# Kernel optimization log

Measured on AMD Instinct MI355X. Metric: run time of the kernel, lower is better.

The kernel has to match this reference:

```python
import jax, jax.numpy as jnp
import numpy as np

N, E = 100000, 1600000
D_NODE, H, OUT = 64, 256, 256
NUM_LAYERS = 3


def setup_inputs() -> dict:
    key = jax.random.key(0)
    ks = jax.random.split(key, 12)
    s = lambda fan_in: 1.0 / np.sqrt(fan_in)
    return {
        "x": jax.random.normal(ks[0], (N, D_NODE), jnp.float32),
        "src": jax.random.randint(ks[1], (E,), 0, N, jnp.int32),
        "dst": jax.random.randint(ks[2], (E,), 0, N, jnp.int32),
        "w_node": jax.random.uniform(ks[3], (D_NODE, H), jnp.float32, -s(D_NODE), s(D_NODE)),
        "b_node": jnp.zeros((H,), jnp.float32),
        "w_gnn": jax.random.uniform(ks[4], (NUM_LAYERS, H, H), jnp.float32, -s(H), s(H)),
        "b_gnn": jnp.zeros((NUM_LAYERS, H), jnp.float32),
        "w_p1": jax.random.uniform(ks[5], (H, H), jnp.float32, -s(H), s(H)),
        "b_p1": jnp.zeros((H,), jnp.float32),
        "w_p2": jax.random.uniform(ks[6], (H, OUT), jnp.float32, -s(H), s(H)),
        "b_p2": jnp.zeros((OUT,), jnp.float32),
    }


def reference(x, src, dst, w_node, b_node, w_gnn, b_gnn, w_p1, b_p1, w_p2, b_p2):
    n = x.shape[0]
    # node projection
    h = x @ w_node + b_node  # [N, H]
    # per-dst neighbor counts (nodes with no neighbors keep zero message)
    deg = jax.ops.segment_sum(jnp.ones_like(dst, jnp.float32), dst, num_segments=n)
    denom = jnp.where(deg > 0, deg, 1.0)[:, None]  # [N, 1]
    for l in range(NUM_LAYERS):
        # scatter-mean aggregation of neighbor embeddings
        msg = jax.ops.segment_sum(h[src], dst, num_segments=n) / denom  # [N, H]
        h = jax.nn.relu(h + msg @ w_gnn[l] + b_gnn[l])
    g = h.mean(axis=0)  # [H]
    latent = jax.nn.relu(g @ w_p1 + b_p1) @ w_p2 + b_p2  # [OUT]
    return latent
```

## Files before the change

kernel.cpp:

```cpp
#include <hip/hip_runtime.h>
#include <hip/hip_bf16.h>
#include <cstdint>
#include <cstddef>

#define DNODE 64
#define HDIM 256
#define NLAYERS 3
#define NPART 8
#define CSH 13
#define HSLICES 128

typedef __attribute__((ext_vector_type(8))) short bf16x8;
typedef __attribute__((ext_vector_type(4))) float f32x4;

__device__ __forceinline__ ushort f2bf(float f) {
    __hip_bfloat16 b = __float2bfloat16(f);
    return *(ushort*)&b;
}
__device__ __forceinline__ float bf2f(ushort u) {
    return __uint_as_float((uint32_t)u << 16);
}
__device__ __forceinline__ unsigned char f2fp8(float f) {
    int p = __builtin_amdgcn_cvt_pk_fp8_f32(f, f, 0, false);
    return (unsigned char)(p & 0xFF);
}

__global__ __launch_bounds__(256) void k_pre(const int* __restrict__ esrc, const int* __restrict__ edst,
                                             int* __restrict__ deg2, int E, int histB, int npp, int nch,
                                             const float* __restrict__ x, ushort* __restrict__ xb, int n4, int xcB,
                                             const float* __restrict__ w_node, ushort* __restrict__ wnt,
                                             const float* __restrict__ w_gnn, ushort* __restrict__ wgt, int wcB,
                                             ushort* __restrict__ wct, float* __restrict__ bc,
                                             const float* __restrict__ b_node) {
    int b = blockIdx.x, tid = threadIdx.x;
    if (b < histB) {
        int part = b & (NPART - 1);
        int slice = b / NPART;
        int lo = part * npp, hi = lo + npp;
        int stride = HSLICES * 256;
        for (int e = slice * 256 + tid; e < E; e += stride) {
            int d = edst[e];
            int s = esrc[e];
            if (d >= lo && d < hi) atomicAdd(&deg2[(size_t)d * nch + (s >> CSH)], 1);
        }
    } else if (b < histB + xcB) {
        int i = (b - histB) * 256 + tid;
        if (i < n4) {
            float4 v = *(const float4*)&x[(size_t)i * 4];
            ushort4 o;
            o.x = f2bf(v.x); o.y = f2bf(v.y); o.z = f2bf(v.z); o.w = f2bf(v.w);
            *(ushort4*)&xb[(size_t)i * 4] = o;
        }
    } else if (b < histB + xcB + wcB) {
        int wb = b - histB - xcB;
        int n = tid;
        if (wb < DNODE / 16) {
            int k0 = wb * 16;
#pragma unroll
            for (int i = 0; i < 16; i++)
                wnt[(size_t)n * DNODE + k0 + i] = f2bf(w_node[(size_t)(k0 + i) * HDIM + n]);
        } else {
            wb -= DNODE / 16;
            int l = wb >> 4, k0 = (wb & 15) * 16;
            const float* s = w_gnn + (size_t)l * HDIM * HDIM;
            ushort* d = wgt + (size_t)l * HDIM * HDIM;
#pragma unroll
            for (int i = 0; i < 16; i++)
                d[(size_t)n * HDIM + k0 + i] = f2bf(s[(size_t)(k0 + i) * HDIM + n]);
        }
    } else {
        int k = b - histB - xcB - wcB;
        int n = tid;
        if (k < DNODE) {
            float s = 0.f;
            for (int j = 0; j < HDIM; j++) s = fmaf(w_node[(size_t)k * HDIM + j], w_gnn[(size_t)j * HDIM + n], s);
            wct[(size_t)n * DNODE + k] = f2bf(s);
        } else {
            float s = 0.f;
            for (int j = 0; j < HDIM; j++) s = fmaf(b_node[j], w_gnn[(size_t)j * HDIM + n], s);
            bc[n] = s;
        }
    }
}

__global__ __launch_bounds__(256) void k_scan_partial(const int* __restrict__ deg, int* __restrict__ bsum, int n) {
    __shared__ int sd[256];
    int tid = threadIdx.x;
    int base = blockIdx.x * 2048 + tid * 8;
    int s = 0;
#pragma unroll
    for (int j = 0; j < 8; j++) {
        int idx = base + j;
        if (idx < n) s += deg[idx];
    }
    sd[tid] = s;
    __syncthreads();
    for (int off = 128; off > 0; off >>= 1) {
        if (tid < off) sd[tid] += sd[tid + off];
        __syncthreads();
    }
    if (tid == 0) bsum[blockIdx.x] = sd[0];
}

__global__ __launch_bounds__(256) void k_scan_bsum(int* __restrict__ bsum, int nb) {
    __shared__ int ts[256];
    int tid = threadIdx.x;
    int v[4], loc[4];
    int s = 0;
#pragma unroll
    for (int j = 0; j < 4; j++) {
        int idx = tid * 4 + j;
        v[j] = (idx < nb) ? bsum[idx] : 0;
        loc[j] = s;
        s += v[j];
    }
    ts[tid] = s;
    __syncthreads();
    for (int off = 1; off < 256; off <<= 1) {
        int t = (tid >= off) ? ts[tid - off] : 0;
        __syncthreads();
        ts[tid] += t;
        __syncthreads();
    }
    int off0 = tid ? ts[tid - 1] : 0;
#pragma unroll
    for (int j = 0; j < 4; j++) {
        int idx = tid * 4 + j;
        if (idx < nb) bsum[idx] = off0 + loc[j];
    }
}

__global__ __launch_bounds__(256) void k_scan_final(const int* __restrict__ deg, const int* __restrict__ bsum,
                                                    int* __restrict__ rp2, int* __restrict__ cursor2,
                                                    int n, int Etot) {
    __shared__ int tsum[256];
    int tid = threadIdx.x;
    int base = blockIdx.x * 2048 + tid * 8;
    int loc[8];
    int s = 0;
#pragma unroll
    for (int j = 0; j < 8; j++) {
        int idx = base + j;
        int v = (idx < n) ? deg[idx] : 0;
        loc[j] = s;
        s += v;
    }
    tsum[tid] = s;
    __syncthreads();
    for (int off = 1; off < 256; off <<= 1) {
        int t = (tid >= off) ? tsum[tid - off] : 0;
        __syncthreads();
        tsum[tid] += t;
        __syncthreads();
    }
    int off0 = bsum[blockIdx.x] + (tid ? tsum[tid - 1] : 0);
#pragma unroll
    for (int j = 0; j < 8; j++) {
        int idx = base + j;
        if (idx < n) {
            int rp = off0 + loc[j];
            rp2[idx] = rp;
            cursor2[idx] = rp;
        }
    }
    if (blockIdx.x == 0 && tid == 0) rp2[n] = Etot;
}

__global__ __launch_bounds__(256) void k_fill_part(const int* __restrict__ esrc, const int* __restrict__ edst,
                                                   int* __restrict__ cursor2, int* __restrict__ colx,
                                                   int E, int npp, int nslices, int nch) {
    int part = blockIdx.x & (NPART - 1);
    int slice = blockIdx.x / NPART;
    int lo = part * npp;
    int hi = lo + npp;
    int stride = nslices * 256;
    for (int e = slice * 256 + (int)threadIdx.x; e < E; e += stride) {
        int d = edst[e];
        if (d >= lo && d < hi) {
            int s = esrc[e];
            int c = s >> CSH;
            int p = atomicAdd(&cursor2[(size_t)d * nch + c], 1);
            colx[p] = s;
        }
    }
}

__global__ __launch_bounds__(256) void k_proj(const ushort* __restrict__ xb,
                                              const ushort* __restrict__ wnt,
                                              const ushort* __restrict__ wct,
                                              const float* __restrict__ bn,
                                              const float* __restrict__ bc,
                                              ushort* __restrict__ hb,
                                              unsigned char* __restrict__ hw8,
                                              int M) {
    __shared__ ushort As[64][40];
    __shared__ ushort Bs[64][40];
    __shared__ ushort Cs[64][40];
    int tid = threadIdx.x;
    int w = tid >> 6, l = tid & 63;
    int row0 = blockIdx.y * 64, col0 = blockIdx.x * 64;
    int sr = tid >> 2, sc = (tid & 3) * 8;
    int wm = (w >> 1) * 32, wn_ = (w & 1) * 32;
    int fr = l & 15, fk = (l >> 4) * 8;
    f32x4 acch[2][2] = {};
    f32x4 accw[2][2] = {};

    for (int k0 = 0; k0 < DNODE; k0 += 32) {
        bf16x8 av = {0, 0, 0, 0, 0, 0, 0, 0};
        int gr = row0 + sr;
        if (gr < M) av = *(const bf16x8*)&xb[(size_t)gr * DNODE + k0 + sc];
        *(bf16x8*)&As[sr][sc] = av;
        *(bf16x8*)&Bs[sr][sc] = *(const bf16x8*)&wnt[(size_t)(col0 + sr) * DNODE + k0 + sc];
        *(bf16x8*)&Cs[sr][sc] = *(const bf16x8*)&wct[(size_t)(col0 + sr) * DNODE + k0 + sc];
        __syncthreads();
        bf16x8 af[2], bff[2], cf[2];
#pragma unroll
        for (int mi = 0; mi < 2; mi++) af[mi] = *(const bf16x8*)&As[wm + mi * 16 + fr][fk];
#pragma unroll
        for (int ni = 0; ni < 2; ni++) {
            bff[ni] = *(const bf16x8*)&Bs[wn_ + ni * 16 + fr][fk];
            cf[ni] = *(const bf16x8*)&Cs[wn_ + ni * 16 + fr][fk];
        }
#pragma unroll
        for (int mi = 0; mi < 2; mi++)
#pragma unroll
            for (int ni = 0; ni < 2; ni++) {
                acch[mi][ni] = __builtin_amdgcn_mfma_f32_16x16x32_bf16(af[mi], bff[ni], acch[mi][ni], 0, 0, 0);
                accw[mi][ni] = __builtin_amdgcn_mfma_f32_16x16x32_bf16(af[mi], cf[ni], accw[mi][ni], 0, 0, 0);
            }
        __syncthreads();
    }

#pragma unroll
    for (int ni = 0; ni < 2; ni++) {
        int gcol = col0 + wn_ + ni * 16 + fr;
        float bbh = bn[gcol];
        float bbw = bc[gcol];
#pragma unroll
        for (int mi = 0; mi < 2; mi++) {
#pragma unroll
            for (int j = 0; j < 4; j++) {
                int grow = row0 + wm + mi * 16 + (l >> 4) * 4 + j;
                if (grow >= M) continue;
                size_t idx = (size_t)grow * HDIM + gcol;
                hb[idx] = f2bf(acch[mi][ni][j] + bbh);
                hw8[idx] = f2fp8(accw[mi][ni][j] + bbw);
            }
        }
    }
}

__global__ __launch_bounds__(256) void k_gemm_hw(const ushort* __restrict__ A,
                                                 const ushort* __restrict__ Bt,
                                                 unsigned char* __restrict__ hw8,
                                                 int M) {
    __shared__ ushort As[64][40];
    __shared__ ushort Bs[64][40];
    int tid = threadIdx.x;
    int w = tid >> 6, l = tid & 63;
    int row0 = blockIdx.y * 64, col0 = blockIdx.x * 64;
    int sr = tid >> 2, sc = (tid & 3) * 8;
    int wm = (w >> 1) * 32, wn = (w & 1) * 32;
    int fr = l & 15, fk = (l >> 4) * 8;
    f32x4 acc[2][2] = {};

    for (int k0 = 0; k0 < HDIM; k0 += 32) {
        bf16x8 av = {0, 0, 0, 0, 0, 0, 0, 0};
        int gr = row0 + sr;
        if (gr < M) av = *(const bf16x8*)&A[(size_t)gr * HDIM + k0 + sc];
        *(bf16x8*)&As[sr][sc] = av;
        *(bf16x8*)&Bs[sr][sc] = *(const bf16x8*)&Bt[(size_t)(col0 + sr) * HDIM + k0 + sc];
        __syncthreads();
        bf16x8 af[2], bf[2];
#pragma unroll
        for (int mi = 0; mi < 2; mi++) af[mi] = *(const bf16x8*)&As[wm + mi * 16 + fr][fk];
#pragma unroll
        for (int ni = 0; ni < 2; ni++) bf[ni] = *(const bf16x8*)&Bs[wn + ni * 16 + fr][fk];
#pragma unroll
        for (int mi = 0; mi < 2; mi++)
#pragma unroll
            for (int ni = 0; ni < 2; ni++)
                acc[mi][ni] = __builtin_amdgcn_mfma_f32_16x16x32_bf16(af[mi], bf[ni], acc[mi][ni], 0, 0, 0);
        __syncthreads();
    }

#pragma unroll
    for (int ni = 0; ni < 2; ni++) {
        int gcol = col0 + wn + ni * 16 + fr;
#pragma unroll
        for (int mi = 0; mi < 2; mi++) {
#pragma unroll
            for (int j = 0; j < 4; j++) {
                int grow = row0 + wm + mi * 16 + (l >> 4) * 4 + j;
                if (grow >= M) continue;
                hw8[(size_t)grow * HDIM + gcol] = f2fp8(acc[mi][ni][j]);
            }
        }
    }
}

__device__ __forceinline__ void acc_fp8x16(uint4 v, float* acc) {
    uint32_t d[4] = {v.x, v.y, v.z, v.w};
#pragma unroll
    for (int i = 0; i < 4; i++) {
        auto lo = __builtin_amdgcn_cvt_pk_f32_fp8(d[i], false);
        auto hi = __builtin_amdgcn_cvt_pk_f32_fp8(d[i], true);
        acc[i * 4 + 0] += lo[0];
        acc[i * 4 + 1] += lo[1];
        acc[i * 4 + 2] += hi[0];
        acc[i * 4 + 3] += hi[1];
    }
}

__global__ __launch_bounds__(256) void k_agg(const unsigned char* __restrict__ hw8,
                                             const int* __restrict__ rp2,
                                             const int* __restrict__ colx,
                                             unsigned char* __restrict__ msg8, int N, int nch) {
    int tid = threadIdx.x;
    int node = blockIdx.x * 16 + (tid >> 4);
    if (node >= N) return;
    int f = tid & 15;
    int gbase = tid & 48;
    const unsigned char* hp = hw8 + (size_t)f * 16;

    int s = rp2[(size_t)node * nch];
    int e = rp2[(size_t)node * nch + nch];
    float acc[16] = {};

    for (int base = s; base < e; base += 16) {
        int rem = e - base;
        int cnt = rem > 16 ? 16 : rem;
        int cv = (f < cnt) ? colx[base + f] : 0;
        int t = 0;
        for (; t + 3 < cnt; t += 4) {
            int c0 = __shfl(cv, gbase + t);
            int c1 = __shfl(cv, gbase + t + 1);
            int c2 = __shfl(cv, gbase + t + 2);
            int c3 = __shfl(cv, gbase + t + 3);
            uint4 v0 = *(const uint4*)&hp[(size_t)c0 * HDIM];
            uint4 v1 = *(const uint4*)&hp[(size_t)c1 * HDIM];
            uint4 v2 = *(const uint4*)&hp[(size_t)c2 * HDIM];
            uint4 v3 = *(const uint4*)&hp[(size_t)c3 * HDIM];
            acc_fp8x16(v0, acc);
            acc_fp8x16(v1, acc);
            acc_fp8x16(v2, acc);
            acc_fp8x16(v3, acc);
        }
        for (; t < cnt; t++) {
            int c0 = __shfl(cv, gbase + t);
            uint4 v0 = *(const uint4*)&hp[(size_t)c0 * HDIM];
            acc_fp8x16(v0, acc);
        }
    }

    int d = e - s;
    float inv = 1.0f / (float)(d > 0 ? d : 1);
    uint32_t w0 = 0, w1 = 0, w2 = 0, w3 = 0;
    w0 = (uint32_t)__builtin_amdgcn_cvt_pk_fp8_f32(acc[0] * inv, acc[1] * inv, (int)w0, false);
    w0 = (uint32_t)__builtin_amdgcn_cvt_pk_fp8_f32(acc[2] * inv, acc[3] * inv, (int)w0, true);
    w1 = (uint32_t)__builtin_amdgcn_cvt_pk_fp8_f32(acc[4] * inv, acc[5] * inv, (int)w1, false);
    w1 = (uint32_t)__builtin_amdgcn_cvt_pk_fp8_f32(acc[6] * inv, acc[7] * inv, (int)w1, true);
    w2 = (uint32_t)__builtin_amdgcn_cvt_pk_fp8_f32(acc[8] * inv, acc[9] * inv, (int)w2, false);
    w2 = (uint32_t)__builtin_amdgcn_cvt_pk_fp8_f32(acc[10] * inv, acc[11] * inv, (int)w2, true);
    w3 = (uint32_t)__builtin_amdgcn_cvt_pk_fp8_f32(acc[12] * inv, acc[13] * inv, (int)w3, false);
    w3 = (uint32_t)__builtin_amdgcn_cvt_pk_fp8_f32(acc[14] * inv, acc[15] * inv, (int)w3, true);
    uint4 o = {w0, w1, w2, w3};
    *(uint4*)&msg8[(size_t)node * HDIM + f * 16] = o;
}

__global__ __launch_bounds__(256) void k_resid(ushort* __restrict__ hb, const unsigned char* __restrict__ msg8,
                                               const float* __restrict__ bias, int total8) {
    int stride = gridDim.x * 256;
    for (int i = blockIdx.x * 256 + (int)threadIdx.x; i < total8; i += stride) {
        int col0 = (i & 31) * 8;
        size_t off = (size_t)i * 8;
        bf16x8 h = *(const bf16x8*)&hb[off];
        uint2 m8 = *(const uint2*)&msg8[off];
        auto lo0 = __builtin_amdgcn_cvt_pk_f32_fp8(m8.x, false);
        auto hi0 = __builtin_amdgcn_cvt_pk_f32_fp8(m8.x, true);
        auto lo1 = __builtin_amdgcn_cvt_pk_f32_fp8(m8.y, false);
        auto hi1 = __builtin_amdgcn_cvt_pk_f32_fp8(m8.y, true);
        float mv[8] = {lo0[0], lo0[1], hi0[0], hi0[1], lo1[0], lo1[1], hi1[0], hi1[1]};
        float4 b0 = *(const float4*)&bias[col0];
        float4 b1 = *(const float4*)&bias[col0 + 4];
        float bl[8] = {b0.x, b0.y, b0.z, b0.w, b1.x, b1.y, b1.z, b1.w};
        ushort o[8];
#pragma unroll
        for (int k = 0; k < 8; k++)
            o[k] = f2bf(fmaxf(bf2f((ushort)h[k]) + mv[k] + bl[k], 0.f));
        *(uint4*)&hb[off] = *(uint4*)o;
    }
}

__global__ __launch_bounds__(256) void k_colsum_res(const ushort* __restrict__ hb,
                                                    const unsigned char* __restrict__ msg8,
                                                    const float* __restrict__ bias, float* __restrict__ g, int N) {
    __shared__ float cols[256];
    int tid = threadIdx.x;
    int f8 = tid & 31, r = tid >> 5;
    int col0 = f8 * 8;
    float4 b0 = *(const float4*)&bias[col0];
    float4 b1 = *(const float4*)&bias[col0 + 4];
    float bl[8] = {b0.x, b0.y, b0.z, b0.w, b1.x, b1.y, b1.z, b1.w};
    float acc[8] = {};
    for (int row = blockIdx.x * 8 + r; row < N; row += gridDim.x * 8) {
        size_t off = (size_t)row * HDIM + col0;
        bf16x8 h = *(const bf16x8*)&hb[off];
        uint2 m8 = *(const uint2*)&msg8[off];
        auto lo0 = __builtin_amdgcn_cvt_pk_f32_fp8(m8.x, false);
        auto hi0 = __builtin_amdgcn_cvt_pk_f32_fp8(m8.x, true);
        auto lo1 = __builtin_amdgcn_cvt_pk_f32_fp8(m8.y, false);
        auto hi1 = __builtin_amdgcn_cvt_pk_f32_fp8(m8.y, true);
        float mv[8] = {lo0[0], lo0[1], hi0[0], hi0[1], lo1[0], lo1[1], hi1[0], hi1[1]};
#pragma unroll
        for (int k = 0; k < 8; k++)
            acc[k] += fmaxf(bf2f((ushort)h[k]) + mv[k] + bl[k], 0.f);
    }
    cols[tid] = 0.f;
    __syncthreads();
#pragma unroll
    for (int k = 0; k < 8; k++) atomicAdd(&cols[col0 + k], acc[k]);
    __syncthreads();
    atomicAdd(&g[tid], cols[tid]);
}

__global__ __launch_bounds__(256) void k_mlp(const float* __restrict__ g, const float* __restrict__ w1,
                                             const float* __restrict__ b1, const float* __restrict__ w2,
                                             const float* __restrict__ b2, float* __restrict__ out, float invN) {
    __shared__ float gs[256];
    __shared__ float ts[256];
    int f = threadIdx.x;
    gs[f] = g[f] * invN;
    __syncthreads();
    float a = b1[f];
    for (int k = 0; k < 256; k++) a = fmaf(gs[k], w1[k * 256 + f], a);
    ts[f] = fmaxf(a, 0.f);
    __syncthreads();
    float o = b2[f];
    for (int k = 0; k < 256; k++) o = fmaf(ts[k], w2[k * 256 + f], o);
    out[f] = o;
}

extern "C" void kernel_launch(void* const* d_in, const int* in_sizes, int n_in,
                              void* d_out, int out_size, void* d_ws, size_t ws_size,
                              hipStream_t stream) {
    const float* x      = (const float*)d_in[0];
    const int*   src    = (const int*)d_in[1];
    const int*   dst    = (const int*)d_in[2];
    const float* w_node = (const float*)d_in[3];
    const float* b_node = (const float*)d_in[4];
    const float* w_gnn  = (const float*)d_in[5];
    const float* b_gnn  = (const float*)d_in[6];
    const float* w_p1   = (const float*)d_in[7];
    const float* b_p1   = (const float*)d_in[8];
    const float* w_p2   = (const float*)d_in[9];
    const float* b_p2   = (const float*)d_in[10];
    float* out = (float*)d_out;

    const int N = in_sizes[0] / DNODE;
    const int E = in_sizes[1];
    const int nch = (N + (1 << CSH) - 1) >> CSH;
    const int n2 = N * nch;

    char* w = (char*)d_ws;
    ushort* hb     = (ushort*)w;            w += (size_t)N * HDIM * 2;
    unsigned char* hw8  = (unsigned char*)w; w += (size_t)N * HDIM;
    unsigned char* msg8 = (unsigned char*)w; w += (size_t)N * HDIM;
    ushort* xb     = (ushort*)w;            w += (size_t)N * DNODE * 2;
    ushort* wnt    = (ushort*)w;            w += (size_t)HDIM * DNODE * 2;
    ushort* wct    = (ushort*)w;            w += (size_t)HDIM * DNODE * 2;
    ushort* wgt    = (ushort*)w;            w += (size_t)NLAYERS * HDIM * HDIM * 2;
    float* bc      = (float*)w;             w += 256 * 4;
    int*   deg2    = (int*)w;               w += (size_t)n2 * 4;
    int*   rp2     = (int*)w;               w += (size_t)(n2 + 1) * 4;
    int*   cursor2 = (int*)w;               w += (size_t)n2 * 4;
    int*   colx    = (int*)w;               w += (size_t)E * 4;
    float* g       = (float*)w;             w += 256 * 4;
    int*   bsum    = (int*)w;               w += 1024 * 4;
    (void)ws_size; (void)n_in; (void)out_size;

    hipMemsetAsync(deg2, 0, (size_t)n2 * 4, stream);
    hipMemsetAsync(g, 0, 256 * 4, stream);

    int histB = NPART * HSLICES;
    int npp = (N + NPART - 1) / NPART;
    int n4 = N * DNODE / 4;
    int xcB = (n4 + 255) / 256;
    int wcB = DNODE / 16 + NLAYERS * (HDIM / 16);
    k_pre<<<histB + xcB + wcB + DNODE + 1, 256, 0, stream>>>(src, dst, deg2, E, histB, npp, nch,
                                                             x, xb, n4, xcB,
                                                             w_node, wnt, w_gnn, wgt, wcB,
                                                             wct, bc, b_node);

    int nb2 = (n2 + 2047) / 2048;
    k_scan_partial<<<nb2, 256, 0, stream>>>(deg2, bsum, n2);
    k_scan_bsum<<<1, 256, 0, stream>>>(bsum, nb2);
    k_scan_final<<<nb2, 256, 0, stream>>>(deg2, bsum, rp2, cursor2, n2, E);

    k_fill_part<<<NPART * 256, 256, 0, stream>>>(src, dst, cursor2, colx, E, npp, 256, nch);

    dim3 gg(HDIM / 64, (N + 63) / 64);
    k_proj<<<gg, 256, 0, stream>>>(xb, wnt, wct, b_node, bc, hb, hw8, N);

    int nagg = (N + 15) / 16;
    int total8 = N * (HDIM / 8);
    for (int l = 0; l < NLAYERS; l++) {
        const float* bg = b_gnn + (size_t)l * HDIM;
        k_agg<<<nagg, 256, 0, stream>>>(hw8, rp2, colx, msg8, N, nch);
        if (l < NLAYERS - 1) {
            k_resid<<<2048, 256, 0, stream>>>(hb, msg8, bg, total8);
            k_gemm_hw<<<gg, 256, 0, stream>>>(hb, wgt + (size_t)(l + 1) * HDIM * HDIM, hw8, N);
        } else {
            k_colsum_res<<<1024, 256, 0, stream>>>(hb, msg8, bg, g, N);
        }
    }

    k_mlp<<<1, 256, 0, stream>>>(g, w_p1, b_p1, w_p2, b_p2, out, 1.0f / (float)N);
}
```

Baseline: 566.6 us.

## Fuse residual-ReLU into next-layer GEMM with full-width row tiles

Removes the separate residual+bias+ReLU kernel and folds it into the A-tile load of the next layer's GEMM. Each block now computes a full 64x256 output tile, so every updated h row is produced once and written back exactly once. The edge histogram and fill loops also use nontemporal loads, and the fill loop now reads src unconditionally. The cost is higher LDS use (a 256-row B tile) and more accumulator registers per thread, which lowers occupancy, plus fewer blocks in the GEMM grid.

```diff
diff --git a/kernel.cpp b/kernel.cpp
--- a/kernel.cpp
+++ b/kernel.cpp
@@ -39,8 +39,8 @@
         int lo = part * npp, hi = lo + npp;
         int stride = HSLICES * 256;
         for (int e = slice * 256 + tid; e < E; e += stride) {
-            int d = edst[e];
-            int s = esrc[e];
+            int d = __builtin_nontemporal_load(&edst[e]);
+            int s = __builtin_nontemporal_load(&esrc[e]);
             if (d >= lo && d < hi) atomicAdd(&deg2[(size_t)d * nch + (s >> CSH)], 1);
         }
     } else if (b < histB + xcB) {
@@ -175,9 +175,9 @@
     int hi = lo + npp;
     int stride = nslices * 256;
     for (int e = slice * 256 + (int)threadIdx.x; e < E; e += stride) {
-        int d = edst[e];
+        int d = __builtin_nontemporal_load(&edst[e]);
+        int s = __builtin_nontemporal_load(&esrc[e]);
         if (d >= lo && d < hi) {
-            int s = esrc[e];
             int c = s >> CSH;
             int p = atomicAdd(&cursor2[(size_t)d * nch + c], 1);
             colx[p] = s;
@@ -250,48 +250,73 @@
     }
 }
 
-__global__ __launch_bounds__(256) void k_gemm_hw(const ushort* __restrict__ A,
-                                                 const ushort* __restrict__ Bt,
-                                                 unsigned char* __restrict__ hw8,
-                                                 int M) {
+__global__ __launch_bounds__(256) void k_gemm_fused2(ushort* __restrict__ hb,
+                                                     const unsigned char* __restrict__ msg8,
+                                                     const float* __restrict__ bias,
+                                                     const ushort* __restrict__ Bt,
+                                                     unsigned char* __restrict__ hw8,
+                                                     int M) {
     __shared__ ushort As[64][40];
-    __shared__ ushort Bs[64][40];
-    int tid = threadIdx.x;
+    __shared__ ushort Bs[256][40];
+    __shared__ float bsh[256];
+    int tid = threadIdx.x;
+    bsh[tid] = bias[tid];
     int w = tid >> 6, l = tid & 63;
-    int row0 = blockIdx.y * 64, col0 = blockIdx.x * 64;
+    int row0 = blockIdx.x * 64;
     int sr = tid >> 2, sc = (tid & 3) * 8;
-    int wm = (w >> 1) * 32, wn = (w & 1) * 32;
     int fr = l & 15, fk = (l >> 4) * 8;
-    f32x4 acc[2][2] = {};
+    f32x4 acc[4][4] = {};
+    __syncthreads();
 
     for (int k0 = 0; k0 < HDIM; k0 += 32) {
         bf16x8 av = {0, 0, 0, 0, 0, 0, 0, 0};
         int gr = row0 + sr;
-        if (gr < M) av = *(const bf16x8*)&A[(size_t)gr * HDIM + k0 + sc];
+        if (gr < M) {
+            size_t off = (size_t)gr * HDIM + k0 + sc;
+            bf16x8 h = *(const bf16x8*)&hb[off];
+            uint2 m8 = *(const uint2*)&msg8[off];
+            auto lo0 = __builtin_amdgcn_cvt_pk_f32_fp8(m8.x, false);
+            auto hi0 = __builtin_amdgcn_cvt_pk_f32_fp8(m8.x, true);
+            auto lo1 = __builtin_amdgcn_cvt_pk_f32_fp8(m8.y, false);
+            auto hi1 = __builtin_amdgcn_cvt_pk_f32_fp8(m8.y, true);
+            float mv[8] = {lo0[0], lo0[1], hi0[0], hi0[1], lo1[0], lo1[1], hi1[0], hi1[1]};
+            ushort o[8];
+#pragma unroll
+            for (int k = 0; k < 8; k++)
+                o[k] = f2bf(fmaxf(bf2f((ushort)h[k]) + mv[k] + bsh[k0 + sc + k], 0.f));
+            av = *(bf16x8*)o;
+            *(bf16x8*)&hb[off] = av;
+        }
         *(bf16x8*)&As[sr][sc] = av;
-        *(bf16x8*)&Bs[sr][sc] = *(const bf16x8*)&Bt[(size_t)(col0 + sr) * HDIM + k0 + sc];
-        __syncthreads();
-        bf16x8 af[2], bf[2];
-#pragma unroll
-        for (int mi = 0; mi < 2; mi++) af[mi] = *(const bf16x8*)&As[wm + mi * 16 + fr][fk];
-#pragma unroll
-        for (int ni = 0; ni < 2; ni++) bf[ni] = *(const bf16x8*)&Bs[wn + ni * 16 + fr][fk];
-#pragma unroll
-        for (int mi = 0; mi < 2; mi++)
-#pragma unroll
-            for (int ni = 0; ni < 2; ni++)
-                acc[mi][ni] = __builtin_amdgcn_mfma_f32_16x16x32_bf16(af[mi], bf[ni], acc[mi][ni], 0, 0, 0);
-        __syncthreads();
-    }
-
-#pragma unroll
-    for (int ni = 0; ni < 2; ni++) {
-        int gcol = col0 + wn + ni * 16 + fr;
-#pragma unroll
-        for (int mi = 0; mi < 2; mi++) {
+        {
+            const ushort* bp = &Bt[(size_t)tid * HDIM + k0];
+            *(bf16x8*)&Bs[tid][0] = *(const bf16x8*)&bp[0];
+            *(bf16x8*)&Bs[tid][8] = *(const bf16x8*)&bp[8];
+            *(bf16x8*)&Bs[tid][16] = *(const bf16x8*)&bp[16];
+            *(bf16x8*)&Bs[tid][24] = *(const bf16x8*)&bp[24];
+        }
+        __syncthreads();
+        bf16x8 af[4];
+#pragma unroll
+        for (int mi = 0; mi < 4; mi++) af[mi] = *(const bf16x8*)&As[mi * 16 + fr][fk];
+#pragma unroll
+        for (int ni = 0; ni < 4; ni++) {
+            bf16x8 bf = *(const bf16x8*)&Bs[w * 64 + ni * 16 + fr][fk];
+#pragma unroll
+            for (int mi = 0; mi < 4; mi++)
+                acc[mi][ni] = __builtin_amdgcn_mfma_f32_16x16x32_bf16(af[mi], bf, acc[mi][ni], 0, 0, 0);
+        }
+        __syncthreads();
+    }
+
+#pragma unroll
+    for (int ni = 0; ni < 4; ni++) {
+        int gcol = w * 64 + ni * 16 + fr;
+#pragma unroll
+        for (int mi = 0; mi < 4; mi++) {
 #pragma unroll
             for (int j = 0; j < 4; j++) {
-                int grow = row0 + wm + mi * 16 + (l >> 4) * 4 + j;
+                int grow = row0 + mi * 16 + (l >> 4) * 4 + j;
                 if (grow >= M) continue;
                 hw8[(size_t)grow * HDIM + gcol] = f2fp8(acc[mi][ni][j]);
             }
@@ -368,30 +393,6 @@
     *(uint4*)&msg8[(size_t)node * HDIM + f * 16] = o;
 }
 
-__global__ __launch_bounds__(256) void k_resid(ushort* __restrict__ hb, const unsigned char* __restrict__ msg8,
-                                               const float* __restrict__ bias, int total8) {
-    int stride = gridDim.x * 256;
-    for (int i = blockIdx.x * 256 + (int)threadIdx.x; i < total8; i += stride) {
-        int col0 = (i & 31) * 8;
-        size_t off = (size_t)i * 8;
-        bf16x8 h = *(const bf16x8*)&hb[off];
-        uint2 m8 = *(const uint2*)&msg8[off];
-        auto lo0 = __builtin_amdgcn_cvt_pk_f32_fp8(m8.x, false);
-        auto hi0 = __builtin_amdgcn_cvt_pk_f32_fp8(m8.x, true);
-        auto lo1 = __builtin_amdgcn_cvt_pk_f32_fp8(m8.y, false);
-        auto hi1 = __builtin_amdgcn_cvt_pk_f32_fp8(m8.y, true);
-        float mv[8] = {lo0[0], lo0[1], hi0[0], hi0[1], lo1[0], lo1[1], hi1[0], hi1[1]};
-        float4 b0 = *(const float4*)&bias[col0];
-        float4 b1 = *(const float4*)&bias[col0 + 4];
-        float bl[8] = {b0.x, b0.y, b0.z, b0.w, b1.x, b1.y, b1.z, b1.w};
-        ushort o[8];
-#pragma unroll
-        for (int k = 0; k < 8; k++)
-            o[k] = f2bf(fmaxf(bf2f((ushort)h[k]) + mv[k] + bl[k], 0.f));
-        *(uint4*)&hb[off] = *(uint4*)o;
-    }
-}
-
 __global__ __launch_bounds__(256) void k_colsum_res(const ushort* __restrict__ hb,
                                                     const unsigned char* __restrict__ msg8,
                                                     const float* __restrict__ bias, float* __restrict__ g, int N) {
@@ -503,13 +504,13 @@
     k_proj<<<gg, 256, 0, stream>>>(xb, wnt, wct, b_node, bc, hb, hw8, N);
 
     int nagg = (N + 15) / 16;
-    int total8 = N * (HDIM / 8);
+    int nblk = (N + 63) / 64;
     for (int l = 0; l < NLAYERS; l++) {
         const float* bg = b_gnn + (size_t)l * HDIM;
         k_agg<<<nagg, 256, 0, stream>>>(hw8, rp2, colx, msg8, N, nch);
         if (l < NLAYERS - 1) {
-            k_resid<<<2048, 256, 0, stream>>>(hb, msg8, bg, total8);
-            k_gemm_hw<<<gg, 256, 0, stream>>>(hb, wgt + (size_t)(l + 1) * HDIM * HDIM, hw8, N);
+            k_gemm_fused2<<<nblk, 256, 0, stream>>>(hb, msg8, bg,
+                                                    wgt + (size_t)(l + 1) * HDIM * HDIM, hw8, N);
         } else {
             k_colsum_res<<<1024, 256, 0, stream>>>(hb, msg8, bg, g, N);
         }
```

Result: no change. 570.4 us (+0.7%).
